# Kernel tuning notes

Hardware: AMD Instinct MI355X
Metric: run time of the kernel (lower is better)

The kernel has to match this reference:

```python
import jax, jax.numpy as jnp
import numpy as np

N = 100000   # n_nodes
E = 1600000  # n_edges per sparse matrix
D = 64       # feature dim
TAU = 0.5
ITERS = 10


def setup_inputs() -> dict:
    key = jax.random.key(0)
    ks = jax.random.split(key, 10)
    A_row = jax.random.randint(ks[0], (E,), 0, N, dtype=jnp.int32)
    A_col = jax.random.randint(ks[1], (E,), 0, N, dtype=jnp.int32)
    A_val = jax.random.uniform(ks[2], (E,), dtype=jnp.float32)
    L_row = jax.random.randint(ks[3], (E,), 0, N, dtype=jnp.int32)
    L_col = jax.random.randint(ks[4], (E,), 0, N, dtype=jnp.int32)
    L_val = jax.random.normal(ks[5], (E,), dtype=jnp.float32)
    embed = jax.random.normal(ks[6], (N, D), dtype=jnp.float32)
    # xavier-ish scale for d x d linears (bias=False per source)
    scale = float(np.sqrt(2.0 / (D + D)))
    W1 = jax.random.normal(ks[7], (D, D), dtype=jnp.float32) * scale
    W2 = jax.random.normal(ks[8], (D, D), dtype=jnp.float32) * scale
    Ws = jax.random.normal(ks[9], (1, D), dtype=jnp.float32) * scale
    return {"A_row": A_row, "A_col": A_col, "A_val": A_val,
            "L_row": L_row, "L_col": L_col, "L_val": L_val,
            "embed": embed, "W1": W1, "W2": W2, "Ws": Ws}


def _spmm(row, col, val, X):
    # COO sparse @ dense: gather X rows by col, scale, scatter-add by row.
    return jax.ops.segment_sum(val[:, None] * X[col], row, num_segments=N)


def reference(A_row, A_col, A_val, L_row, L_col, L_val, embed, W1, W2, Ws):
    X = embed
    for W in (W1, W2):  # L=2 residual directed GNN layers
        AX = _spmm(A_row, A_col, A_val, X)        # [N, D]
        H = jax.nn.relu(AX @ W.T)                 # Linear(bias=False), dropout=0
        X = X + H
    s = X @ Ws.T                                   # [N, 1] scores

    def body(_, v):
        v = _spmm(L_row, L_col, L_val, v)          # [N, 1]
        v = v - TAU * jnp.sign(v)
        norm = jnp.sqrt(jnp.sum(v * v, axis=0, keepdims=True))
        return v / jnp.maximum(norm, 1e-12)        # F.normalize(dim=0)

    v = jax.lax.fori_loop(0, ITERS, body, s)
    return v.squeeze(-1)                           # [N]
```

## Files before the change

kernel.cpp:

```cpp
#include <hip/hip_runtime.h>
#include <hip/hip_bf16.h>
#include <math.h>

#define TAU 0.5f
#define RPB 256
#define SEG 4608
#define CHUNK 8192

__global__ void init_kernel(int* __restrict__ cur, float* __restrict__ norms,
                            int K, int NN) {
    int k = blockIdx.x * 256 + threadIdx.x;
    if (k < K) cur[k] = 0;
    if (k < NN) norms[k] = 0.f;
}

__global__ __launch_bounds__(512)
void bin3_kernel(const int* __restrict__ rowA, const int* __restrict__ colA,
                 const float* __restrict__ valA,
                 const int* __restrict__ rowL, const int* __restrict__ colL,
                 const float* __restrict__ valL,
                 int* __restrict__ cur, int2* __restrict__ tmp,
                 int E, int cblocks, int NBC) {
    __shared__ int cnt[512];
    __shared__ int sbase[512];
    int b = blockIdx.x;
    const int* row;
    const int* col;
    const float* val;
    int koff;
    if (b < cblocks) {
        row = rowA; col = colA; val = valA; koff = 0;
    } else {
        row = rowL; col = colL; val = valL; koff = NBC;
        b -= cblocks;
    }
    int t = threadIdx.x;
    for (int i = t; i < 512; i += 512) cnt[i] = 0;
    __syncthreads();
    int e0 = b * CHUNK;
    int e1 = min(e0 + CHUNK, E);
    for (int e = e0 + t; e < e1; e += 512)
        atomicAdd(&cnt[row[e] >> 8], 1);
    __syncthreads();
    if (t < NBC) {
        int c = cnt[t];
        sbase[t] = c ? atomicAdd(&cur[koff + t], c) : 0;
    }
    __syncthreads();
    for (int i = t; i < 512; i += 512) cnt[i] = 0;
    __syncthreads();
    for (int e = e0 + t; e < e1; e += 512) {
        int r = row[e];
        int bk = r >> 8;
        int rank = atomicAdd(&cnt[bk], 1);
        int pos = sbase[bk] + rank;
        if (pos < SEG)
            tmp[(size_t)(koff + bk) * SEG + pos] =
                make_int2(col[e] | ((r & 255) << 20), __float_as_int(val[e]));
    }
}

__global__ __launch_bounds__(1024)
void scan_kernel(const int* __restrict__ cur, int* __restrict__ boff, int NB2) {
    __shared__ int sh[1024];
    int t = threadIdx.x;
    int c = (t < NB2) ? min(cur[t], SEG) : 0;
    sh[t] = c;
    __syncthreads();
    for (int off = 1; off < 1024; off <<= 1) {
        int x = (t >= off) ? sh[t - off] : 0;
        __syncthreads();
        sh[t] += x;
        __syncthreads();
    }
    if (t < NB2) boff[t] = sh[t] - c;
}

__global__ __launch_bounds__(256)
void place_kernel(const int* __restrict__ cur,
                  const int* __restrict__ boff,
                  const int2* __restrict__ tmp,
                  int* __restrict__ rpA, int* __restrict__ rpL,
                  int2* __restrict__ cvA, int2* __restrict__ cvL,
                  int n, int NBC) {
    int b = blockIdx.x;
    int m = (b >= NBC) ? 1 : 0;
    int lb = b - m * NBC;
    int r0 = lb * RPB;
    int r1 = min(r0 + RPB, n);
    int* rp = m ? rpL : rpA;
    int2* cv = m ? cvL : cvA;
    int lbase = m ? boff[NBC] : 0;
    int p0 = boff[b] - lbase;
    __shared__ int cnt[RPB], curs[RPB], rbase[RPB];
    __shared__ int2 stage[SEG];
    int t = threadIdx.x;
    if (t < RPB) cnt[t] = 0;
    __syncthreads();
    int fill = min(cur[b], SEG);
    const int2* src = tmp + (size_t)b * SEG;
    for (int i = t; i < fill; i += 256) {
        int2 e = src[i];
        stage[i] = e;
        atomicAdd(&cnt[(e.x >> 20) & (RPB - 1)], 1);
    }
    __syncthreads();
    if (t < 64) {
        int base = t * 4;
        int loc[4];
        int s = 0;
#pragma unroll
        for (int j = 0; j < 4; ++j) { loc[j] = s; s += cnt[base + j]; }
        int sc = s;
#pragma unroll
        for (int off = 1; off < 64; off <<= 1) {
            int y = __shfl_up(sc, off, 64);
            if (t >= off) sc += y;
        }
        int ex = sc - s;
#pragma unroll
        for (int j = 0; j < 4; ++j) {
            rbase[base + j] = ex + loc[j];
            curs[base + j] = ex + loc[j];
        }
    }
    __syncthreads();
    if (t < r1 - r0) rp[r0 + t] = p0 + rbase[t];
    if (t == 0 && lb == NBC - 1) rp[n] = p0 + fill;
    __syncthreads();
    for (int i = t; i < fill; i += 256) {
        int2 e = stage[i];
        int pos = atomicAdd(&curs[(e.x >> 20) & (RPB - 1)], 1);
        cv[p0 + pos] = make_int2(e.x & 0xFFFFF, e.y);
    }
}

__global__ void fused_layer_kernel(const int* __restrict__ row_ptr,
                                   const int2* __restrict__ cv,
                                   const float* __restrict__ X,
                                   const float* __restrict__ W,
                                   float* __restrict__ Xn,
                                   float* __restrict__ s,
                                   const float* __restrict__ Wsv, int n) {
    __shared__ float Wt[64 * 68];
    int tid = threadIdx.x;
    for (int i = tid; i < 4096; i += 256) {
        int j = i >> 6, k = i & 63;
        Wt[k * 68 + j] = W[i];
    }
    __syncthreads();
    int lane = tid & 63;
    int ql = lane & 15;
    int q = lane >> 4;
    int wv = tid >> 6;
    float4 ws4 = {0.f, 0.f, 0.f, 0.f};
    if (s != nullptr) ws4 = *(const float4*)&Wsv[4 * ql];
    int rbase = (blockIdx.x * 4 + wv) * 4;
    if (rbase >= n) return;
    int row = rbase + q;
    bool act = row < n;
    int rr = act ? row : 0;
    int p0 = row_ptr[rr];
    int end = act ? row_ptr[rr + 1] : p0;
    float4 a0 = {0.f, 0.f, 0.f, 0.f}, a1 = {0.f, 0.f, 0.f, 0.f};
    float4 a2 = {0.f, 0.f, 0.f, 0.f}, a3 = {0.f, 0.f, 0.f, 0.f};
    int p = p0;
    for (; p + 3 < end; p += 4) {
        int2 e0 = cv[p], e1 = cv[p + 1], e2 = cv[p + 2], e3 = cv[p + 3];
        float4 x0 = *(const float4*)&X[(size_t)e0.x * 64 + 4 * ql];
        float4 x1 = *(const float4*)&X[(size_t)e1.x * 64 + 4 * ql];
        float4 x2 = *(const float4*)&X[(size_t)e2.x * 64 + 4 * ql];
        float4 x3 = *(const float4*)&X[(size_t)e3.x * 64 + 4 * ql];
        float v0 = __int_as_float(e0.y), v1 = __int_as_float(e1.y);
        float v2 = __int_as_float(e2.y), v3 = __int_as_float(e3.y);
        a0.x += v0 * x0.x; a0.y += v0 * x0.y; a0.z += v0 * x0.z; a0.w += v0 * x0.w;
        a1.x += v1 * x1.x; a1.y += v1 * x1.y; a1.z += v1 * x1.z; a1.w += v1 * x1.w;
        a2.x += v2 * x2.x; a2.y += v2 * x2.y; a2.z += v2 * x2.z; a2.w += v2 * x2.w;
        a3.x += v3 * x3.x; a3.y += v3 * x3.y; a3.z += v3 * x3.z; a3.w += v3 * x3.w;
    }
    for (; p < end; ++p) {
        int2 e = cv[p];
        float4 x = *(const float4*)&X[(size_t)e.x * 64 + 4 * ql];
        float v = __int_as_float(e.y);
        a0.x += v * x.x; a0.y += v * x.y; a0.z += v * x.z; a0.w += v * x.w;
    }
    float4 acc;
    acc.x = (a0.x + a1.x) + (a2.x + a3.x);
    acc.y = (a0.y + a1.y) + (a2.y + a3.y);
    acc.z = (a0.z + a1.z) + (a2.z + a3.z);
    acc.w = (a0.w + a1.w) + (a2.w + a3.w);
    float4 h4 = {0.f, 0.f, 0.f, 0.f};
    int qb = 16 * q;
#pragma unroll
    for (int kk = 0; kk < 64; kk += 4) {
        int src = qb + (kk >> 2);
        float b0 = __shfl(acc.x, src, 64);
        float b1 = __shfl(acc.y, src, 64);
        float b2 = __shfl(acc.z, src, 64);
        float b3 = __shfl(acc.w, src, 64);
        float4 w0 = *(const float4*)&Wt[(kk + 0) * 68 + 4 * ql];
        float4 w1 = *(const float4*)&Wt[(kk + 1) * 68 + 4 * ql];
        float4 w2 = *(const float4*)&Wt[(kk + 2) * 68 + 4 * ql];
        float4 w3 = *(const float4*)&Wt[(kk + 3) * 68 + 4 * ql];
        h4.x += b0 * w0.x + b1 * w1.x + b2 * w2.x + b3 * w3.x;
        h4.y += b0 * w0.y + b1 * w1.y + b2 * w2.y + b3 * w3.y;
        h4.z += b0 * w0.z + b1 * w1.z + b2 * w2.z + b3 * w3.z;
        h4.w += b0 * w0.w + b1 * w1.w + b2 * w2.w + b3 * w3.w;
    }
    if (act) {
        float4 xv = *(const float4*)&X[(size_t)row * 64 + 4 * ql];
        float4 o;
        o.x = xv.x + fmaxf(h4.x, 0.f);
        o.y = xv.y + fmaxf(h4.y, 0.f);
        o.z = xv.z + fmaxf(h4.z, 0.f);
        o.w = xv.w + fmaxf(h4.w, 0.f);
        *(float4*)&Xn[(size_t)row * 64 + 4 * ql] = o;
        if (s != nullptr) {
            float d = o.x * ws4.x + o.y * ws4.y + o.z * ws4.z + o.w * ws4.w;
#pragma unroll
            for (int off = 8; off; off >>= 1) d += __shfl_down(d, off, 16);
            if (ql == 0) s[row] = d;
        }
    }
}

__global__ void power_iter_kernel(const int* __restrict__ row_ptr,
                                  const int2* __restrict__ cv,
                                  const float* __restrict__ v_in,
                                  float* __restrict__ v_out,
                                  const float* __restrict__ norm_prev,
                                  float* __restrict__ norm_out,
                                  int n) {
    int lane = threadIdx.x & 63;
    float scale = 1.f;
    if (norm_prev) {
        float x = norm_prev[lane];
#pragma unroll
        for (int off = 32; off; off >>= 1) x += __shfl_xor(x, off, 64);
        scale = 1.f / fmaxf(sqrtf(x), 1e-12f);
    }
    int g = blockIdx.x * 256 + threadIdx.x;
    int row = g >> 1;
    int t = g & 1;
    float sq = 0.f;
    if (row < n) {
        int p = row_ptr[row] + t;
        int end = row_ptr[row + 1];
        float s0 = 0.f, s1 = 0.f, s2 = 0.f, s3 = 0.f;
        for (; p + 6 < end; p += 8) {
            int2 e0 = cv[p], e1 = cv[p + 2], e2 = cv[p + 4], e3 = cv[p + 6];
            s0 += __int_as_float(e0.y) * v_in[e0.x];
            s1 += __int_as_float(e1.y) * v_in[e1.x];
            s2 += __int_as_float(e2.y) * v_in[e2.x];
            s3 += __int_as_float(e3.y) * v_in[e3.x];
        }
        for (; p < end; p += 2) {
            int2 e = cv[p];
            s0 += __int_as_float(e.y) * v_in[e.x];
        }
        float sv = (s0 + s1) + (s2 + s3);
        sv += __shfl_xor(sv, 1, 2);
        if (t == 0) {
            float sg = (sv > 0.f) ? 1.f : ((sv < 0.f) ? -1.f : 0.f);
            float w = sv * scale - TAU * sg;
            v_out[row] = w;
            sq = w * w;
        }
    }
    for (int off = 32; off; off >>= 1) sq += __shfl_down(sq, off, 64);
    __shared__ float sh[4];
    int wv = threadIdx.x >> 6;
    if (lane == 0) sh[wv] = sq;
    __syncthreads();
    if (threadIdx.x == 0)
        atomicAdd(&norm_out[blockIdx.x & 63], sh[0] + sh[1] + sh[2] + sh[3]);
}

__global__ void finalize_kernel(const float* __restrict__ v,
                                const float* __restrict__ slots,
                                float* __restrict__ out, int n) {
    int lane = threadIdx.x & 63;
    float x = slots[lane];
#pragma unroll
    for (int off = 32; off; off >>= 1) x += __shfl_xor(x, off, 64);
    float inv = 1.f / fmaxf(sqrtf(x), 1e-12f);
    int i = blockIdx.x * 256 + threadIdx.x;
    if (i < n) out[i] = v[i] * inv;
}

extern "C" void kernel_launch(void* const* d_in, const int* in_sizes, int n_in,
                              void* d_out, int out_size, void* d_ws, size_t ws_size,
                              hipStream_t stream) {
    const int* A_row = (const int*)d_in[0];
    const int* A_col = (const int*)d_in[1];
    const float* A_val = (const float*)d_in[2];
    const int* L_row = (const int*)d_in[3];
    const int* L_col = (const int*)d_in[4];
    const float* L_val = (const float*)d_in[5];
    const float* embed = (const float*)d_in[6];
    const float* W1 = (const float*)d_in[7];
    const float* W2 = (const float*)d_in[8];
    const float* Ws = (const float*)d_in[9];
    float* out = (float*)d_out;

    const int E = in_sizes[0];
    const int D = 64;
    const int N = in_sizes[6] / D;
    const int ITERS = 10;
    const int NBC = (N + RPB - 1) / RPB;
    const int NB2 = 2 * NBC;
    const int cblocks = (E + CHUNK - 1) / CHUNK;

    char* ws = (char*)d_ws;
    size_t off = 0;
    auto carve = [&](size_t bytes) {
        void* p = ws + off;
        off += (bytes + 255) & ~(size_t)255;
        return p;
    };
    size_t feat_bytes = (size_t)N * D * sizeof(float);
    size_t tmp_bytes = (size_t)NB2 * SEG * sizeof(int2);
    char* base = (char*)carve(tmp_bytes > 2 * feat_bytes ? tmp_bytes : 2 * feat_bytes);
    float* X0 = (float*)base;
    float* X1 = (float*)(base + feat_bytes);
    int2* tmp = (int2*)base;
    int* A_rp = (int*)carve((size_t)(N + 1) * sizeof(int));
    int2* A_cv = (int2*)carve((size_t)E * sizeof(int2));
    int* L_rp = (int*)carve((size_t)(N + 1) * sizeof(int));
    int2* L_cv = (int2*)carve((size_t)E * sizeof(int2));
    int* cur = (int*)carve((size_t)NB2 * sizeof(int));
    int* boff = (int*)carve((size_t)NB2 * sizeof(int));
    float* v_cur = (float*)carve((size_t)N * sizeof(float));
    float* v_new = (float*)carve((size_t)N * sizeof(float));
    float* norms = (float*)carve((size_t)ITERS * 64 * sizeof(float));

    int imax = NB2 > ITERS * 64 ? NB2 : ITERS * 64;
    init_kernel<<<(imax + 255) / 256, 256, 0, stream>>>(cur, norms, NB2, ITERS * 64);
    bin3_kernel<<<2 * cblocks, 512, 0, stream>>>(A_row, A_col, A_val,
                                                 L_row, L_col, L_val,
                                                 cur, tmp, E, cblocks, NBC);
    scan_kernel<<<1, 1024, 0, stream>>>(cur, boff, NB2);
    place_kernel<<<NB2, 256, 0, stream>>>(cur, boff, tmp,
                                          A_rp, L_rp, A_cv, L_cv, N, NBC);

    int fl_blocks = (N + 15) / 16;
    fused_layer_kernel<<<fl_blocks, 256, 0, stream>>>(
        A_rp, A_cv, embed, W1, X0, nullptr, Ws, N);
    fused_layer_kernel<<<fl_blocks, 256, 0, stream>>>(
        A_rp, A_cv, X0, W2, X1, v_cur, Ws, N);

    int p_blocks = (N * 2 + 255) / 256;
    int n_blocks = (N + 255) / 256;
    float* cur_v = v_cur;
    float* nxt_v = v_new;
    for (int it = 0; it < ITERS; ++it) {
        power_iter_kernel<<<p_blocks, 256, 0, stream>>>(
            L_rp, L_cv, cur_v, nxt_v,
            it ? (norms + (it - 1) * 64) : nullptr, norms + it * 64, N);
        float* t = cur_v; cur_v = nxt_v; nxt_v = t;
    }
    finalize_kernel<<<n_blocks, 256, 0, stream>>>(cur_v, norms + (ITERS - 1) * 64, out, N);
}
```

Measured before the change: 522.7 us.

## Fuse power iterations into one persistent kernel with grid-wide atomic barrier

Replaces the ten separate power-iteration launches with a single persistent kernel that loops over the iterations. It keeps row bounds in registers and synchronises all blocks between iterations through an atomic counter barrier with acquire/release semantics and s_sleep backoff. This removes per-iteration launch gaps and repeated row_ptr loads. The cost is a spin barrier over about 782 blocks contending on one counter. It also relies on every block being co-resident, which launch_bounds(256,4) is meant to ensure; if any block is not resident, the kernel deadlocks.

```diff
diff --git a/kernel.cpp b/kernel.cpp
--- a/kernel.cpp
+++ b/kernel.cpp
@@ -224,56 +224,73 @@
     }
 }
 
-__global__ void power_iter_kernel(const int* __restrict__ row_ptr,
-                                  const int2* __restrict__ cv,
-                                  const float* __restrict__ v_in,
-                                  float* __restrict__ v_out,
-                                  const float* __restrict__ norm_prev,
-                                  float* __restrict__ norm_out,
-                                  int n) {
-    int lane = threadIdx.x & 63;
-    float scale = 1.f;
-    if (norm_prev) {
-        float x = norm_prev[lane];
-#pragma unroll
-        for (int off = 32; off; off >>= 1) x += __shfl_xor(x, off, 64);
-        scale = 1.f / fmaxf(sqrtf(x), 1e-12f);
-    }
-    int g = blockIdx.x * 256 + threadIdx.x;
+__global__ __launch_bounds__(256, 4)
+void power_persist_kernel(const int* __restrict__ row_ptr,
+                          const int2* __restrict__ cv,
+                          float* vA, float* vB,
+                          float* norms,
+                          int* bar,
+                          int n, int iters) {
+    int tid = threadIdx.x;
+    int lane = tid & 63;
+    int wv = tid >> 6;
+    int g = blockIdx.x * 256 + tid;
     int row = g >> 1;
     int t = g & 1;
-    float sq = 0.f;
-    if (row < n) {
-        int p = row_ptr[row] + t;
-        int end = row_ptr[row + 1];
-        float s0 = 0.f, s1 = 0.f, s2 = 0.f, s3 = 0.f;
-        for (; p + 6 < end; p += 8) {
-            int2 e0 = cv[p], e1 = cv[p + 2], e2 = cv[p + 4], e3 = cv[p + 6];
-            s0 += __int_as_float(e0.y) * v_in[e0.x];
-            s1 += __int_as_float(e1.y) * v_in[e1.x];
-            s2 += __int_as_float(e2.y) * v_in[e2.x];
-            s3 += __int_as_float(e3.y) * v_in[e3.x];
-        }
-        for (; p < end; p += 2) {
-            int2 e = cv[p];
-            s0 += __int_as_float(e.y) * v_in[e.x];
-        }
-        float sv = (s0 + s1) + (s2 + s3);
-        sv += __shfl_xor(sv, 1, 2);
-        if (t == 0) {
-            float sg = (sv > 0.f) ? 1.f : ((sv < 0.f) ? -1.f : 0.f);
-            float w = sv * scale - TAU * sg;
-            v_out[row] = w;
-            sq = w * w;
-        }
-    }
-    for (int off = 32; off; off >>= 1) sq += __shfl_down(sq, off, 64);
+    int nblk = gridDim.x;
     __shared__ float sh[4];
-    int wv = threadIdx.x >> 6;
-    if (lane == 0) sh[wv] = sq;
-    __syncthreads();
-    if (threadIdx.x == 0)
-        atomicAdd(&norm_out[blockIdx.x & 63], sh[0] + sh[1] + sh[2] + sh[3]);
+    int p0 = 0, end = 0;
+    if (row < n) { p0 = row_ptr[row] + t; end = row_ptr[row + 1]; }
+    for (int it = 0; it < iters; ++it) {
+        const float* v_in = (it & 1) ? vB : vA;
+        float* v_out = (it & 1) ? vA : vB;
+        float scale = 1.f;
+        if (it > 0) {
+            float x = norms[(it - 1) * 64 + lane];
+#pragma unroll
+            for (int off = 32; off; off >>= 1) x += __shfl_xor(x, off, 64);
+            scale = 1.f / fmaxf(sqrtf(x), 1e-12f);
+        }
+        float sq = 0.f;
+        if (row < n) {
+            float s0 = 0.f, s1 = 0.f, s2 = 0.f, s3 = 0.f;
+            int p = p0;
+            for (; p + 6 < end; p += 8) {
+                int2 e0 = cv[p], e1 = cv[p + 2], e2 = cv[p + 4], e3 = cv[p + 6];
+                s0 += __int_as_float(e0.y) * v_in[e0.x];
+                s1 += __int_as_float(e1.y) * v_in[e1.x];
+                s2 += __int_as_float(e2.y) * v_in[e2.x];
+                s3 += __int_as_float(e3.y) * v_in[e3.x];
+            }
+            for (; p < end; p += 2) {
+                int2 e = cv[p];
+                s0 += __int_as_float(e.y) * v_in[e.x];
+            }
+            float sv = (s0 + s1) + (s2 + s3);
+            sv += __shfl_xor(sv, 1, 2);
+            if (t == 0) {
+                float sg = (sv > 0.f) ? 1.f : ((sv < 0.f) ? -1.f : 0.f);
+                float w = sv * scale - TAU * sg;
+                v_out[row] = w;
+                sq = w * w;
+            }
+        }
+        for (int off = 32; off; off >>= 1) sq += __shfl_down(sq, off, 64);
+        if (lane == 0) sh[wv] = sq;
+        __syncthreads();
+        if (tid == 0) {
+            atomicAdd(&norms[it * 64 + (blockIdx.x & 63)],
+                      sh[0] + sh[1] + sh[2] + sh[3]);
+            __threadfence();
+            __hip_atomic_fetch_add(&bar[it], 1, __ATOMIC_RELEASE,
+                                   __HIP_MEMORY_SCOPE_AGENT);
+            while (__hip_atomic_load(&bar[it], __ATOMIC_ACQUIRE,
+                                     __HIP_MEMORY_SCOPE_AGENT) < nblk)
+                __builtin_amdgcn_s_sleep(8);
+            __threadfence();
+        }
+        __syncthreads();
+    }
 }
 
 __global__ void finalize_kernel(const float* __restrict__ v,
@@ -332,10 +349,12 @@
     int* boff = (int*)carve((size_t)NB2 * sizeof(int));
     float* v_cur = (float*)carve((size_t)N * sizeof(float));
     float* v_new = (float*)carve((size_t)N * sizeof(float));
-    float* norms = (float*)carve((size_t)ITERS * 64 * sizeof(float));
-
-    int imax = NB2 > ITERS * 64 ? NB2 : ITERS * 64;
-    init_kernel<<<(imax + 255) / 256, 256, 0, stream>>>(cur, norms, NB2, ITERS * 64);
+    float* norms = (float*)carve(((size_t)ITERS * 64 + 64) * sizeof(float));
+    int* bar = (int*)(norms + ITERS * 64);
+
+    int nzero = ITERS * 64 + 64;
+    int imax = NB2 > nzero ? NB2 : nzero;
+    init_kernel<<<(imax + 255) / 256, 256, 0, stream>>>(cur, norms, NB2, nzero);
     bin3_kernel<<<2 * cblocks, 512, 0, stream>>>(A_row, A_col, A_val,
                                                  L_row, L_col, L_val,
                                                  cur, tmp, E, cblocks, NBC);
@@ -350,14 +369,9 @@
         A_rp, A_cv, X0, W2, X1, v_cur, Ws, N);
 
     int p_blocks = (N * 2 + 255) / 256;
+    power_persist_kernel<<<p_blocks, 256, 0, stream>>>(
+        L_rp, L_cv, v_cur, v_new, norms, bar, N, ITERS);
     int n_blocks = (N + 255) / 256;
-    float* cur_v = v_cur;
-    float* nxt_v = v_new;
-    for (int it = 0; it < ITERS; ++it) {
-        power_iter_kernel<<<p_blocks, 256, 0, stream>>>(
-            L_rp, L_cv, cur_v, nxt_v,
-            it ? (norms + (it - 1) * 64) : nullptr, norms + it * 64, N);
-        float* t = cur_v; cur_v = nxt_v; nxt_v = t;
-    }
-    finalize_kernel<<<n_blocks, 256, 0, stream>>>(cur_v, norms + (ITERS - 1) * 64, out, N);
-}
+    finalize_kernel<<<n_blocks, 256, 0, stream>>>(
+        v_cur, norms + (ITERS - 1) * 64, out, N);
+}
```

New measurement: 1.870 ms. 258% more time.
